# Kernel tuning notes

Hardware: AMD Instinct MI355X
Metric: run time of the kernel (lower is better)

## Reference

```python
import jax, jax.numpy as jnp
import numpy as np

BS, H, L, D = 16, 16, 4096, 32  # bs, n_heads, seq_len(=q_len), head_dim

def setup_inputs() -> dict:
    key = jax.random.key(0)
    kq, kk, kv = jax.random.split(key, 3)
    q = jax.random.normal(kq, (BS, H, L, D), dtype=jnp.float32)
    k = jax.random.normal(kk, (BS, H, D, L), dtype=jnp.float32)
    v = jax.random.normal(kv, (BS, H, L, D), dtype=jnp.float32)
    return {"q": q, "k": k, "v": v}

def reference(q, k, v):
    # reordered attention: scores = (k @ v) / sqrt(seq_len) -> [bs,h,d_k,d_v]
    seq_len = v.shape[2]
    scores = jnp.einsum('bhds,bhse->bhde', k, v) / jnp.sqrt(jnp.float32(seq_len))
    # faithful to source: softmax over dim=0 (the batch dimension)
    attn_weights = jax.nn.softmax(scores, axis=0)
    # dropout p=0.0 -> identity
    # output = q @ weights -> [bs,h,q_len,d_v]
    output = jnp.einsum('bhld,bhde->bhle', q, attn_weights)
    return output, attn_weights
```

## Files before the change

### kernel.cpp

```cpp
#include <hip/hip_runtime.h>

#define BS 16
#define NH 16
#define LQ 4096
#define DH 32

constexpr size_t OUT_ELEMS = (size_t)BS * NH * LQ * DH;
constexpr int HDE = NH * DH * DH;

__device__ __forceinline__ void fma4(float4& a, float s, const float4& v) {
    a.x = fmaf(s, v.x, a.x);
    a.y = fmaf(s, v.y, a.y);
    a.z = fmaf(s, v.z, a.z);
    a.w = fmaf(s, v.w, a.w);
}

template<int NWIN>
__global__ __launch_bounds__(64) void kv_partial(const float* __restrict__ k,
                                                 const float* __restrict__ v,
                                                 float* __restrict__ part) {
    __shared__ float kt[1024];
    __shared__ float vt[1024];
    const int l  = threadIdx.x;
    const int nsplit = 128 / NWIN;
    const int p  = blockIdx.x % nsplit;
    const int bh = blockIdx.x / nsplit;

    const int sp = l >> 5;
    const int dg = (l >> 2) & 7;
    const int eg = l & 3;
    const int d0 = dg << 2;
    const int e0 = eg << 3;

    const float* kb = k + (size_t)bh * DH * LQ;
    const float* vb = v + (size_t)bh * LQ * DH;

    const int krow8 = l >> 3;
    const int kcs   = l & 7;
    const int ksw   = l >> 5;

    float4 acc[4][2];
#pragma unroll
    for (int i = 0; i < 4; ++i) {
        acc[i][0] = make_float4(0.f, 0.f, 0.f, 0.f);
        acc[i][1] = make_float4(0.f, 0.f, 0.f, 0.f);
    }

#pragma unroll
    for (int c = 0; c < NWIN; ++c) {
        const int wb = (p * NWIN + c) << 5;

        float4 kst[4], vst[4];
#pragma unroll
        for (int j = 0; j < 4; ++j) {
            const int r    = (j << 3) + krow8;
            const int csrc = kcs ^ (((j << 1) + ksw) & 7);
            kst[j] = *(const float4*)(kb + (size_t)r * LQ + wb + (csrc << 2));
        }
#pragma unroll
        for (int j = 0; j < 4; ++j) {
            const int s = (j << 3) + krow8;
            vst[j] = *(const float4*)(vb + ((size_t)(wb + s) << 5) + (kcs << 2));
        }
#pragma unroll
        for (int j = 0; j < 4; ++j) *(float4*)(kt + (j << 8) + (l << 2)) = kst[j];
#pragma unroll
        for (int j = 0; j < 4; ++j) *(float4*)(vt + (j << 8) + (l << 2)) = vst[j];
        __builtin_amdgcn_sched_barrier(0);

#pragma unroll
        for (int st = 0; st < 4; ++st) {
            const int cc = (sp << 2) + st;
            float4 kq[4];
#pragma unroll
            for (int i = 0; i < 4; ++i)
                kq[i] = *(const float4*)(kt + ((d0 + i) << 5) + (((cc ^ dg) & 7) << 2));
#pragma unroll
            for (int u = 0; u < 4; ++u) {
                const int s = (cc << 2) + u;
                const float4 vu0 = *(const float4*)(vt + (s << 5) + e0);
                const float4 vu1 = *(const float4*)(vt + (s << 5) + e0 + 4);
#pragma unroll
                for (int i = 0; i < 4; ++i) {
                    const float ks = (u == 0) ? kq[i].x
                                   : (u == 1) ? kq[i].y
                                   : (u == 2) ? kq[i].z : kq[i].w;
                    fma4(acc[i][0], ks, vu0);
                    fma4(acc[i][1], ks, vu1);
                }
            }
        }
        __builtin_amdgcn_sched_barrier(0);
    }

#pragma unroll
    for (int i = 0; i < 4; ++i)
#pragma unroll
        for (int h = 0; h < 2; ++h) {
            acc[i][h].x += __shfl_xor(acc[i][h].x, 32);
            acc[i][h].y += __shfl_xor(acc[i][h].y, 32);
            acc[i][h].z += __shfl_xor(acc[i][h].z, 32);
            acc[i][h].w += __shfl_xor(acc[i][h].w, 32);
        }

    float* pb = part + ((size_t)p << 18) + ((size_t)bh << 10);
#pragma unroll
    for (int i = 0; i < 4; ++i) {
        const float4 wv = (sp == 0) ? acc[i][0] : acc[i][1];
        *(float4*)(pb + ((d0 + i) << 5) + e0 + (sp << 2)) = wv;
    }
}

__global__ __launch_bounds__(256) void reduce_p(const float* __restrict__ part,
                                                float* __restrict__ wts, int nsp) {
    const int gidx = blockIdx.x * 256 + threadIdx.x;
    float s = 0.f;
#pragma unroll 8
    for (int pp = 0; pp < nsp; ++pp)
        s += part[((size_t)pp << 18) + gidx];
    wts[gidx] = s * (1.0f / 64.0f);
}

__global__ __launch_bounds__(256) void softmax_b(float* __restrict__ wts) {
    const int idx = blockIdx.x * 256 + threadIdx.x;

    float sc[BS];
#pragma unroll
    for (int b = 0; b < BS; ++b) sc[b] = wts[((size_t)b << 14) + idx];
    float m = sc[0];
#pragma unroll
    for (int b = 1; b < BS; ++b) m = fmaxf(m, sc[b]);
    float sum = 0.f;
#pragma unroll
    for (int b = 0; b < BS; ++b) { sc[b] = __expf(sc[b] - m); sum += sc[b]; }
    const float inv = 1.0f / sum;
#pragma unroll
    for (int b = 0; b < BS; ++b) wts[((size_t)b << 14) + idx] = sc[b] * inv;
}

__global__ __launch_bounds__(256, 2) void qw(const float* __restrict__ q,
                                             const float* __restrict__ wts,
                                             float* __restrict__ out) {
    __shared__ float qs[128 * 36];
    const int blk = blockIdx.x;
    const int bh  = blk >> 5;
    const int lt  = blk & 31;
    const int tid = threadIdx.x;

    const float* qbase = q + ((size_t)bh * LQ + lt * 128) * DH;

#pragma unroll
    for (int pp = 0; pp < 4; ++pp) {
        const int idx = pp * 256 + tid;
        const int row = idx >> 3;
        const int c4  = idx & 7;
        const float4 t = *(const float4*)(qbase + idx * 4);
        *(float4*)(qs + row * 36 + c4 * 4) = t;
    }

    const int lsub = tid >> 3;
    const int e0   = (tid & 7) << 2;

    const int b = bh >> 4, h = bh & 15;
    float4 Wf[32];
    const float* wbase = wts + ((size_t)b << 14) + ((size_t)h << 10) + e0;
#pragma unroll
    for (int d = 0; d < 32; ++d) Wf[d] = *(const float4*)(wbase + d * DH);

    __syncthreads();

    float* obase = out + ((size_t)bh * LQ + lt * 128) * DH;

#pragma unroll
    for (int r = 0; r < 4; ++r) {
        const int lr = lsub + r * 32;
        const float* qrow = qs + lr * 36;
        float4 acc = {0, 0, 0, 0};
#pragma unroll
        for (int d4 = 0; d4 < 32; d4 += 4) {
            const float4 qv = *(const float4*)(qrow + d4);
            fma4(acc, qv.x, Wf[d4 + 0]);
            fma4(acc, qv.y, Wf[d4 + 1]);
            fma4(acc, qv.z, Wf[d4 + 2]);
            fma4(acc, qv.w, Wf[d4 + 3]);
        }
        *(float4*)(obase + (size_t)lr * DH + e0) = acc;
    }
}

extern "C" void kernel_launch(void* const* d_in, const int* in_sizes, int n_in,
                              void* d_out, int out_size, void* d_ws, size_t ws_size,
                              hipStream_t stream) {
    const float* q = (const float*)d_in[0];
    const float* k = (const float*)d_in[1];
    const float* v = (const float*)d_in[2];
    float* out  = (float*)d_out;
    float* wts  = out + OUT_ELEMS;
    float* part = (float*)d_ws;

    const size_t need32 = (size_t)32 * 256 * 1024 * 4;
    int nsp;
    if (ws_size >= need32) {
        kv_partial<4><<<256 * 32, 64, 0, stream>>>(k, v, part);
        nsp = 32;
    } else {
        kv_partial<16><<<256 * 8, 64, 0, stream>>>(k, v, part);
        nsp = 8;
    }
    reduce_p<<<(BS * HDE) / 256, 256, 0, stream>>>(part, wts, nsp);
    softmax_b<<<HDE / 256, 256, 0, stream>>>(wts);
    qw<<<BS * NH * (LQ / 128), 256, 0, stream>>>(q, wts, out);
}
```

Measured before the change: 141.1 us.

## Double-buffer K/V tiles via async global-to-LDS loads in kv_partial

Rewrites the K·V partial kernel so each 256-thread block runs four independent wavefront tasks. Each wave double-buffers its K/V window tiles in LDS using global_load_lds async copies, so the next window loads while the current one is computed. Each thread now accumulates an 8x8 tile instead of 4x8, with an extra shuffle stage for the reduction. The split count drops from 32 to 16 to cut partial traffic in the reduce step, at the cost of more LDS per block, more registers and longer serial windows per wave.

```diff
diff --git a/kernel.cpp b/kernel.cpp
--- a/kernel.cpp
+++ b/kernel.cpp
@@ -7,6 +7,17 @@
 
 constexpr size_t OUT_ELEMS = (size_t)BS * NH * LQ * DH;
 constexpr int HDE = NH * DH * DH;
+
+__device__ __forceinline__ void async_cp16(float* dst, const float* src) {
+    __builtin_amdgcn_global_load_lds(
+        (const __attribute__((address_space(1))) void*)src,
+        (__attribute__((address_space(3))) void*)dst, 16, 0, 0);
+}
+
+__device__ __forceinline__ void vmfence() {
+    asm volatile("s_waitcnt vmcnt(0)" ::: "memory");
+    __builtin_amdgcn_sched_barrier(0);
+}
 
 __device__ __forceinline__ void fma4(float4& a, float s, const float4& v) {
     a.x = fmaf(s, v.x, a.x);
@@ -16,72 +27,80 @@
 }
 
 template<int NWIN>
-__global__ __launch_bounds__(64) void kv_partial(const float* __restrict__ k,
-                                                 const float* __restrict__ v,
-                                                 float* __restrict__ part) {
-    __shared__ float kt[1024];
-    __shared__ float vt[1024];
-    const int l  = threadIdx.x;
+__global__ __launch_bounds__(256, 2) void kv_partial(const float* __restrict__ k,
+                                                     const float* __restrict__ v,
+                                                     float* __restrict__ part) {
+    __shared__ float lds[16384];
+    const int tid = threadIdx.x;
+    const int w   = tid >> 6;
+    const int l   = tid & 63;
     const int nsplit = 128 / NWIN;
-    const int p  = blockIdx.x % nsplit;
-    const int bh = blockIdx.x / nsplit;
-
-    const int sp = l >> 5;
-    const int dg = (l >> 2) & 7;
+    const int task = blockIdx.x * 4 + w;
+    const int p  = task % nsplit;
+    const int bh = task / nsplit;
+
+    const int sp = l >> 4;
+    const int dg = (l >> 2) & 3;
     const int eg = l & 3;
-    const int d0 = dg << 2;
-    const int e0 = eg << 3;
+    const int d0 = dg << 3;
+    const int e0g = eg << 1;
 
     const float* kb = k + (size_t)bh * DH * LQ;
     const float* vb = v + (size_t)bh * LQ * DH;
-
-    const int krow8 = l >> 3;
-    const int kcs   = l & 7;
-    const int ksw   = l >> 5;
-
-    float4 acc[4][2];
-#pragma unroll
-    for (int i = 0; i < 4; ++i) {
+    float* wlds = lds + (w << 12);
+
+    size_t kgsrc[4], vgsrc[4];
+#pragma unroll
+    for (int j = 0; j < 4; ++j) {
+        const int r = (j << 3) + (l >> 3);
+        kgsrc[j] = (size_t)r * LQ + (((l & 7) ^ j) << 2);
+        const int g = (l & 7) ^ (j + ((l >> 5) << 2));
+        vgsrc[j] = ((size_t)((j << 3) + (l >> 3)) << 5) + (g << 2);
+    }
+
+    float4 acc[8][2];
+#pragma unroll
+    for (int i = 0; i < 8; ++i) {
         acc[i][0] = make_float4(0.f, 0.f, 0.f, 0.f);
         acc[i][1] = make_float4(0.f, 0.f, 0.f, 0.f);
     }
 
+#define FILL(c_) do {                                                          \
+        float* kt_ = wlds + (((c_) & 1) << 11);                                \
+        float* vt_ = kt_ + 1024;                                               \
+        const int wb_ = (p * NWIN + (c_)) << 5;                                \
+        _Pragma("unroll")                                                      \
+        for (int j = 0; j < 4; ++j)                                            \
+            async_cp16(kt_ + (j << 8), kb + kgsrc[j] + wb_);                   \
+        _Pragma("unroll")                                                      \
+        for (int j = 0; j < 4; ++j)                                            \
+            async_cp16(vt_ + (j << 8), vb + vgsrc[j] + ((size_t)wb_ << 5));    \
+    } while (0)
+
+    FILL(0);
+    vmfence();
+
 #pragma unroll
     for (int c = 0; c < NWIN; ++c) {
-        const int wb = (p * NWIN + c) << 5;
-
-        float4 kst[4], vst[4];
-#pragma unroll
-        for (int j = 0; j < 4; ++j) {
-            const int r    = (j << 3) + krow8;
-            const int csrc = kcs ^ (((j << 1) + ksw) & 7);
-            kst[j] = *(const float4*)(kb + (size_t)r * LQ + wb + (csrc << 2));
-        }
-#pragma unroll
-        for (int j = 0; j < 4; ++j) {
-            const int s = (j << 3) + krow8;
-            vst[j] = *(const float4*)(vb + ((size_t)(wb + s) << 5) + (kcs << 2));
-        }
-#pragma unroll
-        for (int j = 0; j < 4; ++j) *(float4*)(kt + (j << 8) + (l << 2)) = kst[j];
-#pragma unroll
-        for (int j = 0; j < 4; ++j) *(float4*)(vt + (j << 8) + (l << 2)) = vst[j];
-        __builtin_amdgcn_sched_barrier(0);
-
-#pragma unroll
-        for (int st = 0; st < 4; ++st) {
-            const int cc = (sp << 2) + st;
-            float4 kq[4];
-#pragma unroll
-            for (int i = 0; i < 4; ++i)
+        if (c + 1 < NWIN) FILL(c + 1);
+
+        const float* kt = wlds + ((c & 1) << 11);
+        const float* vt = kt + 1024;
+#pragma unroll
+        for (int it = 0; it < 2; ++it) {
+            const int cc  = (sp << 1) + it;
+            const int pcc = (cc >> 1) | ((cc & 1) << 2);
+            float4 kq[8];
+#pragma unroll
+            for (int i = 0; i < 8; ++i)
                 kq[i] = *(const float4*)(kt + ((d0 + i) << 5) + (((cc ^ dg) & 7) << 2));
 #pragma unroll
             for (int u = 0; u < 4; ++u) {
                 const int s = (cc << 2) + u;
-                const float4 vu0 = *(const float4*)(vt + (s << 5) + e0);
-                const float4 vu1 = *(const float4*)(vt + (s << 5) + e0 + 4);
-#pragma unroll
-                for (int i = 0; i < 4; ++i) {
+                const float4 vu0 = *(const float4*)(vt + (s << 5) + (((e0g ^ pcc) & 7) << 2));
+                const float4 vu1 = *(const float4*)(vt + (s << 5) + ((((e0g | 1) ^ pcc) & 7) << 2));
+#pragma unroll
+                for (int i = 0; i < 8; ++i) {
                     const float ks = (u == 0) ? kq[i].x
                                    : (u == 1) ? kq[i].y
                                    : (u == 2) ? kq[i].z : kq[i].w;
@@ -90,24 +109,31 @@
                 }
             }
         }
-        __builtin_amdgcn_sched_barrier(0);
-    }
-
-#pragma unroll
-    for (int i = 0; i < 4; ++i)
+        vmfence();
+    }
+#undef FILL
+
+#pragma unroll
+    for (int i = 0; i < 8; ++i)
 #pragma unroll
         for (int h = 0; h < 2; ++h) {
+            acc[i][h].x += __shfl_xor(acc[i][h].x, 16);
+            acc[i][h].y += __shfl_xor(acc[i][h].y, 16);
+            acc[i][h].z += __shfl_xor(acc[i][h].z, 16);
+            acc[i][h].w += __shfl_xor(acc[i][h].w, 16);
             acc[i][h].x += __shfl_xor(acc[i][h].x, 32);
             acc[i][h].y += __shfl_xor(acc[i][h].y, 32);
             acc[i][h].z += __shfl_xor(acc[i][h].z, 32);
             acc[i][h].w += __shfl_xor(acc[i][h].w, 32);
         }
 
-    float* pb = part + ((size_t)p << 18) + ((size_t)bh << 10);
-#pragma unroll
-    for (int i = 0; i < 4; ++i) {
-        const float4 wv = (sp == 0) ? acc[i][0] : acc[i][1];
-        *(float4*)(pb + ((d0 + i) << 5) + e0 + (sp << 2)) = wv;
+    if (sp == 0) {
+        float* pb = part + (((size_t)p << 8) + bh) * 1024;
+#pragma unroll
+        for (int i = 0; i < 8; ++i) {
+            *(float4*)(pb + ((d0 + i) << 5) + (e0g << 2))     = acc[i][0];
+            *(float4*)(pb + ((d0 + i) << 5) + (e0g << 2) + 4) = acc[i][1];
+        }
     }
 }
 
@@ -198,13 +224,13 @@
     float* wts  = out + OUT_ELEMS;
     float* part = (float*)d_ws;
 
-    const size_t need32 = (size_t)32 * 256 * 1024 * 4;
+    const size_t need16 = (size_t)16 * 256 * 1024 * 4;
     int nsp;
-    if (ws_size >= need32) {
-        kv_partial<4><<<256 * 32, 64, 0, stream>>>(k, v, part);
-        nsp = 32;
+    if (ws_size >= need16) {
+        kv_partial<8><<<(256 * 16) / 4, 256, 0, stream>>>(k, v, part);
+        nsp = 16;
     } else {
-        kv_partial<16><<<256 * 8, 64, 0, stream>>>(k, v, part);
+        kv_partial<16><<<(256 * 8) / 4, 256, 0, stream>>>(k, v, part);
         nsp = 8;
     }
     reduce_p<<<(BS * HDE) / 256, 256, 0, stream>>>(part, wts, nsp);
```

Result: no change. 140.9 us (-0.1%).
